# Performance work log

Hardware: AMD Instinct MI355X
Metric: run time of the kernel (lower is better)

The kernel has to match this reference:

```python
import jax, jax.numpy as jnp
import numpy as np

N_NODES = 10000
N_EDGES = 320000
N_GRAPHS = 16


def _sage_layer(h, src, dst, W_self, W_neigh, b):
    # DGL SAGEConv('mean'): out_i = h_i @ W_self + mean_{j in N_in(i)} h_j @ W_neigh + b
    msg_sum = jax.ops.segment_sum(h[src], dst, num_segments=N_NODES)
    deg = jax.ops.segment_sum(jnp.ones(src.shape[0], h.dtype), dst, num_segments=N_NODES)
    h_neigh = msg_sum / jnp.maximum(deg, 1.0)[:, None]
    return h @ W_self + h_neigh @ W_neigh + b


def _segment_mean(x, seg, num_segments):
    s = jax.ops.segment_sum(x, seg, num_segments=num_segments)
    c = jax.ops.segment_sum(jnp.ones(x.shape[0], x.dtype), seg, num_segments=num_segments)
    return s / jnp.maximum(c, 1.0)[:, None]


def setup_inputs() -> dict:
    key = jax.random.key(0)
    ks = jax.random.split(key, 16)
    d_in, d_h, n_cls = 256, 64, 2

    def glorot(k, shape):
        fan_in = shape[0]
        return jax.random.normal(k, shape, dtype=jnp.float32) / np.sqrt(fan_in)

    return {
        "feat": jax.random.normal(ks[0], (N_NODES, d_in), dtype=jnp.float32),
        "src": jax.random.randint(ks[1], (N_EDGES,), 0, N_NODES),
        "dst": jax.random.randint(ks[2], (N_EDGES,), 0, N_NODES),
        "graph_id": jnp.sort(jax.random.randint(ks[3], (N_NODES,), 0, N_GRAPHS)),
        "W_self1": glorot(ks[4], (d_in, d_h)),
        "W_neigh1": glorot(ks[5], (d_in, d_h)),
        "b1": jnp.zeros((d_h,), jnp.float32),
        "W_self2": glorot(ks[6], (d_h, d_h)),
        "W_neigh2": glorot(ks[7], (d_h, d_h)),
        "b2": jnp.zeros((d_h,), jnp.float32),
        "W_self3": glorot(ks[8], (d_h, d_h)),
        "W_neigh3": glorot(ks[9], (d_h, d_h)),
        "b3": jnp.zeros((d_h,), jnp.float32),
        "W_cls": glorot(ks[10], (d_h, n_cls)),
        "b_cls": jnp.zeros((n_cls,), jnp.float32),
    }


def reference(feat, src, dst, graph_id, W_self1, W_neigh1, b1, W_self2, W_neigh2, b2,
              W_self3, W_neigh3, b3, W_cls, b_cls):
    # layer 1 + relu (dropout is identity in eval mode)
    h = jax.nn.relu(_sage_layer(feat, src, dst, W_self1, W_neigh1, b1))
    # layer 2 + relu
    h = jax.nn.relu(_sage_layer(h, src, dst, W_self2, W_neigh2, b2))
    # layer 3 (no activation)
    h = _sage_layer(h, src, dst, W_self3, W_neigh3, b3)
    # dgl.mean_nodes readout per graph
    out_feat = _segment_mean(h, graph_id, N_GRAPHS)
    out = out_feat @ W_cls + b_cls
    return (out, out_feat, h)
```

## Files before the change

kernel.cpp:

```cpp
#include <hip/hip_runtime.h>


#define DH 64
#define NG 16
#define NSB 8
#define DTILES 32
#define MAXNPB 1250
#define CAP 32
#define TILE_F 4352

__device__ __forceinline__ unsigned short f2bf(float f) {
    unsigned int u = __float_as_uint(f);
    unsigned int r = (u + 0x7FFFu + ((u >> 16) & 1u)) >> 16;
    return (unsigned short)r;
}
__device__ __forceinline__ float bfu(unsigned short v) {
    return __uint_as_float(((unsigned int)v) << 16);
}
__device__ __forceinline__ int deg8(const int* __restrict__ cnt8, int n) {
    const int4* cp = reinterpret_cast<const int4*>(&cnt8[n * NSB]);
    int4 c0 = cp[0], c1 = cp[1];
    return c0.x + c0.y + c0.z + c0.w + c1.x + c1.y + c1.z + c1.w;
}

__global__ __launch_bounds__(512) void gemm1_build_kernel(
    const float* __restrict__ X, const float* __restrict__ Ws_g,
    const float* __restrict__ Wn_g, const float* __restrict__ bias,
    float* __restrict__ S, unsigned short* __restrict__ P,
    float* __restrict__ Hn_out,
    const int* __restrict__ src, const int* __restrict__ dst,
    int* __restrict__ cnt8, int* __restrict__ es,
    int M, int E, int npb8, int gb) {
    constexpr int K = 256;
    int tid = threadIdx.x;

    if ((int)blockIdx.x >= gb) {
        int i = ((int)blockIdx.x - gb) * 512 + tid;
        if (i < E) {
            int s = src[i];
            int k = dst[i] * NSB + s / npb8;
            int p = atomicAdd(&cnt8[k], 1);
            if (p < CAP) es[(size_t)k * CAP + p] = s;
        }
        return;
    }

    __shared__ float smem[6 * TILE_F];
    const int grp = tid >> 8;
    const int t   = tid & 255;
    const int cx = t & 15;
    const int ry = t >> 4;
    float* Xs  = smem + grp * 3 * TILE_F;
    float* Wsm = Xs + TILE_F;
    float* Wnm = Wsm + TILE_F;
    const int row0 = blockIdx.x * 64;
    float acc_s[4][4] = {{0.f}};
    float acc_n[4][4] = {{0.f}};

    for (int st = 0; st < 2; ++st) {
        const int kc = grp * 128 + st * 64;
#pragma unroll
        for (int it = 0; it < 4; ++it) {
            int q = t + 256 * it;
            int row = q >> 4;
            int k4 = (q & 15) * 4;
            float4 xv = make_float4(0.f, 0.f, 0.f, 0.f);
            int gr = row0 + row;
            if (gr < M)
                xv = *reinterpret_cast<const float4*>(&X[(size_t)gr * K + kc + k4]);
            *reinterpret_cast<float4*>(&Xs[row * 68 + k4]) = xv;
            *reinterpret_cast<float4*>(&Wsm[row * 68 + k4]) =
                *reinterpret_cast<const float4*>(&Ws_g[(size_t)(kc + row) * 64 + k4]);
            *reinterpret_cast<float4*>(&Wnm[row * 68 + k4]) =
                *reinterpret_cast<const float4*>(&Wn_g[(size_t)(kc + row) * 64 + k4]);
        }
        __syncthreads();
#pragma unroll 4
        for (int kk = 0; kk < 64; ++kk) {
            float av[4], bs[4], bn[4];
#pragma unroll
            for (int j = 0; j < 4; ++j) av[j] = Xs[(ry * 4 + j) * 68 + kk];
#pragma unroll
            for (int i = 0; i < 4; ++i) {
                bs[i] = Wsm[kk * 68 + cx + 16 * i];
                bn[i] = Wnm[kk * 68 + cx + 16 * i];
            }
#pragma unroll
            for (int j = 0; j < 4; ++j)
#pragma unroll
                for (int i = 0; i < 4; ++i) {
                    acc_s[j][i] += av[j] * bs[i];
                    acc_n[j][i] += av[j] * bn[i];
                }
        }
        __syncthreads();
    }

    float* flat = smem + 3 * TILE_F;
    if (grp == 1) {
        int o = t * 33;
#pragma unroll
        for (int j = 0; j < 4; ++j)
#pragma unroll
            for (int i = 0; i < 4; ++i) {
                flat[o + j * 4 + i]      = acc_s[j][i];
                flat[o + 16 + j * 4 + i] = acc_n[j][i];
            }
    }
    __syncthreads();
    if (grp == 0) {
        int o = t * 33;
#pragma unroll
        for (int j = 0; j < 4; ++j)
#pragma unroll
            for (int i = 0; i < 4; ++i) {
                acc_s[j][i] += flat[o + j * 4 + i];
                acc_n[j][i] += flat[o + 16 + j * 4 + i];
            }
#pragma unroll
        for (int j = 0; j < 4; ++j) {
            int r = row0 + ry * 4 + j;
            if (r < M) {
#pragma unroll
                for (int i = 0; i < 4; ++i) {
                    int col = cx + 16 * i;
                    S[(size_t)r * DH + col] = acc_s[j][i] + bias[col];
                    P[(size_t)r * DH + col] = f2bf(acc_n[j][i]);
                    Hn_out[(size_t)r * DH + col] = 0.f;
                }
            }
        }
    }
}

__global__ __launch_bounds__(512) void gemm_dual_kernel(
    const float* __restrict__ X, const float* __restrict__ Ws_g,
    const float* __restrict__ Wn_g, const float* __restrict__ bias,
    const float* __restrict__ Hn_in, const int* __restrict__ cnt8,
    float* __restrict__ S, unsigned short* __restrict__ P,
    float* __restrict__ Hn_out, int M) {
    constexpr int K = 64;
    __shared__ float smem[3 * TILE_F];
    int tid = threadIdx.x;
    const int grp = tid >> 8;
    const int t   = tid & 255;
    const int cx = t & 15;
    const int ry = t >> 4;
    float* Xs  = smem;
    float* Wsm = smem + TILE_F;
    float* Wnm = smem + 2 * TILE_F;
    const int row0 = blockIdx.x * 64;
    float acc_s[4][4] = {{0.f}};
    float acc_n[4][4] = {{0.f}};

    {
#pragma unroll
        for (int it = 0; it < 2; ++it) {
            int q = tid + 512 * it;
            int row = q >> 4;
            int k4 = (q & 15) * 4;
            float4 xv = make_float4(0.f, 0.f, 0.f, 0.f);
            int gr = row0 + row;
            if (gr < M) {
                xv = *reinterpret_cast<const float4*>(&X[(size_t)gr * K + k4]);
                float4 hv = *reinterpret_cast<const float4*>(&Hn_in[(size_t)gr * DH + k4]);
                float inv = 1.f / fmaxf((float)deg8(cnt8, gr), 1.f);
                xv.x = fmaxf(fmaf(hv.x, inv, xv.x), 0.f);
                xv.y = fmaxf(fmaf(hv.y, inv, xv.y), 0.f);
                xv.z = fmaxf(fmaf(hv.z, inv, xv.z), 0.f);
                xv.w = fmaxf(fmaf(hv.w, inv, xv.w), 0.f);
            }
            *reinterpret_cast<float4*>(&Xs[row * 68 + k4]) = xv;
            *reinterpret_cast<float4*>(&Wsm[row * 68 + k4]) =
                *reinterpret_cast<const float4*>(&Ws_g[(size_t)row * 64 + k4]);
            *reinterpret_cast<float4*>(&Wnm[row * 68 + k4]) =
                *reinterpret_cast<const float4*>(&Wn_g[(size_t)row * 64 + k4]);
        }
        __syncthreads();
        const int kk0 = grp * 32;
#pragma unroll 4
        for (int kk = kk0; kk < kk0 + 32; ++kk) {
            float av[4], bs[4], bn[4];
#pragma unroll
            for (int j = 0; j < 4; ++j) av[j] = Xs[(ry * 4 + j) * 68 + kk];
#pragma unroll
            for (int i = 0; i < 4; ++i) {
                bs[i] = Wsm[kk * 68 + cx + 16 * i];
                bn[i] = Wnm[kk * 68 + cx + 16 * i];
            }
#pragma unroll
            for (int j = 0; j < 4; ++j)
#pragma unroll
                for (int i = 0; i < 4; ++i) {
                    acc_s[j][i] += av[j] * bs[i];
                    acc_n[j][i] += av[j] * bn[i];
                }
        }
        __syncthreads();
    }

    if (grp == 1) {
        int o = t * 33;
#pragma unroll
        for (int j = 0; j < 4; ++j)
#pragma unroll
            for (int i = 0; i < 4; ++i) {
                smem[o + j * 4 + i]      = acc_s[j][i];
                smem[o + 16 + j * 4 + i] = acc_n[j][i];
            }
    }
    __syncthreads();
    if (grp == 0) {
        int o = t * 33;
#pragma unroll
        for (int j = 0; j < 4; ++j)
#pragma unroll
            for (int i = 0; i < 4; ++i) {
                acc_s[j][i] += smem[o + j * 4 + i];
                acc_n[j][i] += smem[o + 16 + j * 4 + i];
            }
#pragma unroll
        for (int j = 0; j < 4; ++j) {
            int r = row0 + ry * 4 + j;
            if (r < M) {
#pragma unroll
                for (int i = 0; i < 4; ++i) {
                    int col = cx + 16 * i;
                    S[(size_t)r * DH + col] = acc_s[j][i] + bias[col];
                    P[(size_t)r * DH + col] = f2bf(acc_n[j][i]);
                    Hn_out[(size_t)r * DH + col] = 0.f;
                }
            }
        }
    }
}

__global__ __launch_bounds__(1024) void agg_kernel(
    const unsigned short* __restrict__ P, const int* __restrict__ cnt8,
    const int* __restrict__ es, float* __restrict__ Hn, int M, int npb8) {
    __shared__ __align__(16) unsigned short sP[MAXNPB * DH];
    int tid = threadIdx.x;
    int sb    = blockIdx.x & (NSB - 1);
    int dtile = blockIdx.x >> 3;
    int s0 = sb * npb8;
    int snodes = min(npb8, M - s0);

    {
        const uint4* gp = reinterpret_cast<const uint4*>(P + (size_t)s0 * DH);
        int cnt = snodes * 8;
        for (int j = tid; j < cnt; j += 1024)
            *reinterpret_cast<uint4*>(&sP[j * 8]) = gp[j];
    }
    __syncthreads();

    int lane = tid & 63, wid = tid >> 6;
    int dpb  = (M + DTILES - 1) / DTILES;
    int d0t  = dtile * dpb;
    int dend = min(d0t + dpb, M);

    for (int dstn = d0t + wid; dstn < dend; dstn += 16) {
        int key = dstn * NSB + sb;
        int cnt = min(cnt8[key], CAP);
        if (cnt == 0) continue;
        size_t base = (size_t)key * CAP;
        float acc = 0.f;
        int cmax = cnt - 1;
        for (int e = 0; e < cnt; e += 4) {
            int i0 = es[base + min(e + 0, cmax)] - s0;
            int i1 = es[base + min(e + 1, cmax)] - s0;
            int i2 = es[base + min(e + 2, cmax)] - s0;
            int i3 = es[base + min(e + 3, cmax)] - s0;
            float m1 = (e + 1 < cnt) ? 1.f : 0.f;
            float m2 = (e + 2 < cnt) ? 1.f : 0.f;
            float m3 = (e + 3 < cnt) ? 1.f : 0.f;
            float f0 = bfu(sP[(size_t)i0 * DH + lane]);
            float f1 = bfu(sP[(size_t)i1 * DH + lane]);
            float f2 = bfu(sP[(size_t)i2 * DH + lane]);
            float f3 = bfu(sP[(size_t)i3 * DH + lane]);
            acc += f0;
            acc = fmaf(m1, f1, acc);
            acc = fmaf(m2, f2, acc);
            acc = fmaf(m3, f3, acc);
        }
        atomicAdd(&Hn[(size_t)dstn * DH + lane], acc);
    }
}

__global__ __launch_bounds__(256) void finish_readout_kernel(
    const float* __restrict__ S, const float* __restrict__ Hn,
    const int* __restrict__ cnt8, const int* __restrict__ graph_id,
    float* __restrict__ H, float* __restrict__ gsum, float* __restrict__ gcnt,
    const float* __restrict__ Wc, const float* __restrict__ bc,
    float* __restrict__ out, float* __restrict__ out_feat,
    unsigned int* __restrict__ done, int M, int fb) {
    int tid  = threadIdx.x;
    int lane = tid & 63;
    int wv   = tid >> 6;
    {
        int wid = blockIdx.x * 4 + wv;
        int nw  = fb * 4;
        int cpw = (M + nw - 1) / nw;
        int n0 = wid * cpw, n1 = min(n0 + cpw, M);
        if (n0 < n1) {
            float acc = 0.f;
            int cnt = 0;
            int cur = graph_id[n0];
            for (int n = n0; n < n1; ++n) {
                int gid = graph_id[n];
                if (gid != cur) {
                    atomicAdd(&gsum[cur * DH + lane], acc);
                    if (lane == 0) atomicAdd(&gcnt[cur], (float)cnt);
                    acc = 0.f; cnt = 0; cur = gid;
                }
                float inv = 1.f / fmaxf((float)deg8(cnt8, n), 1.f);
                size_t o = (size_t)n * DH + lane;
                float val = fmaf(Hn[o], inv, S[o]);
                H[o] = val;
                acc += val;
                ++cnt;
            }
            atomicAdd(&gsum[cur * DH + lane], acc);
            if (lane == 0) atomicAdd(&gcnt[cur], (float)cnt);
        }
    }

    __shared__ unsigned int s_ticket;
    __syncthreads();
    if (tid == 0) {
        __threadfence();
        s_ticket = __hip_atomic_fetch_add(done, 1u, __ATOMIC_ACQ_REL,
                                          __HIP_MEMORY_SCOPE_AGENT);
    }
    __syncthreads();
    if (s_ticket != (unsigned int)(fb - 1)) return;
    if (tid == 0) __threadfence();
    __syncthreads();

    __shared__ float ofs[NG][DH];
#pragma unroll
    for (int q = 0; q < 4; ++q) {
        int idx = tid + 256 * q;
        int g = idx >> 6, d = idx & 63;
        float of = gsum[idx] / fmaxf(gcnt[g], 1.0f);
        out_feat[idx] = of;
        ofs[g][d] = of;
    }
    __syncthreads();
    if (tid < NG * 2) {
        int gg = tid >> 1, cc = tid & 1;
        float accv = bc[cc];
#pragma unroll 8
        for (int dd = 0; dd < DH; ++dd) accv += ofs[gg][dd] * Wc[dd * 2 + cc];
        out[gg * 2 + cc] = accv;
    }
}

extern "C" void kernel_launch(void* const* d_in, const int* in_sizes, int n_in,
                              void* d_out, int out_size, void* d_ws, size_t ws_size,
                              hipStream_t stream) {
    const float* feat     = (const float*)d_in[0];
    const int*   src      = (const int*)d_in[1];
    const int*   dst      = (const int*)d_in[2];
    const int*   graph_id = (const int*)d_in[3];
    const float* Ws1 = (const float*)d_in[4];
    const float* Wn1 = (const float*)d_in[5];
    const float* b1  = (const float*)d_in[6];
    const float* Ws2 = (const float*)d_in[7];
    const float* Wn2 = (const float*)d_in[8];
    const float* b2  = (const float*)d_in[9];
    const float* Ws3 = (const float*)d_in[10];
    const float* Wn3 = (const float*)d_in[11];
    const float* b3  = (const float*)d_in[12];
    const float* Wc  = (const float*)d_in[13];
    const float* bc  = (const float*)d_in[14];

    const int M  = in_sizes[3];
    const int E  = in_sizes[1];
    const int M2 = M * NSB;
    const int npb8 = (M + NSB - 1) / NSB;

    float* out      = (float*)d_out;
    float* out_feat = out + NG * 2;
    float* Hbuf     = out_feat + NG * DH;

    char* w = (char*)d_ws;
    size_t off = 0;
    auto carve = [&](size_t bytes) {
        size_t o = off;
        off = (off + bytes + 255) & ~(size_t)255;
        return o;
    };
    int*   cnt8  = (int*)  (w + carve((size_t)M2 * 4));
    float* gsum  = (float*)(w + carve((size_t)NG * DH * 4));
    float* gcnt  = (float*)(w + carve((size_t)NG * 4));
    unsigned int* done = (unsigned int*)(w + carve(4));
    size_t zero_bytes = off;
    int*   es    = (int*)  (w + carve((size_t)M2 * CAP * 4));
    float* Sbuf  = (float*)(w + carve((size_t)M * DH * 4));
    unsigned short* Pbuf = (unsigned short*)(w + carve((size_t)M * DH * 2));
    float* Hn    = (float*)(w + carve((size_t)M * DH * 4));
    (void)ws_size; (void)n_in; (void)out_size;

    (void)hipMemsetAsync(d_ws, 0, zero_bytes, stream);

    int gb = (M + 63) / 64;
    int eb = (E + 511) / 512;
    int ab = NSB * DTILES;
    int fb = 160;

    gemm1_build_kernel<<<gb + eb, 512, 0, stream>>>(
        feat, Ws1, Wn1, b1, Sbuf, Pbuf, Hn,
        src, dst, cnt8, es, M, E, npb8, gb);
    agg_kernel<<<ab, 1024, 0, stream>>>(Pbuf, cnt8, es, Hn, M, npb8);

    gemm_dual_kernel<<<gb, 512, 0, stream>>>(
        Sbuf, Ws2, Wn2, b2, Hn, cnt8, Sbuf, Pbuf, Hn, M);
    agg_kernel<<<ab, 1024, 0, stream>>>(Pbuf, cnt8, es, Hn, M, npb8);

    gemm_dual_kernel<<<gb, 512, 0, stream>>>(
        Sbuf, Ws3, Wn3, b3, Hn, cnt8, Sbuf, Pbuf, Hn, M);
    agg_kernel<<<ab, 1024, 0, stream>>>(Pbuf, cnt8, es, Hn, M, npb8);

    finish_readout_kernel<<<fb, 256, 0, stream>>>(
        Sbuf, Hn, cnt8, graph_id, Hbuf, gsum, gcnt,
        Wc, bc, out, out_feat, done, M, fb);
}
```

Baseline: 233.4 us.

## Replace atomic neighbor accumulation with per-source-bucket partials and 16-bit edge indices

The aggregation kernel now writes one partial sum per (destination, source-bucket) pair with plain stores instead of float atomicAdd into a shared Hn buffer. The consumers (the dual GEMM and the readout) sum the nonzero partials, skipping buckets whose count is zero. This removes the atomics and the zeroing writes of Hn in the GEMM epilogues. Edge source indices are also stored as 16-bit offsets relative to their bucket, halving edge-list traffic. In exchange the partial buffer is eight times larger, and consumers issue up to eight reads per row element.

```diff
diff --git a/kernel.cpp b/kernel.cpp
--- a/kernel.cpp
+++ b/kernel.cpp
@@ -17,19 +17,13 @@
 __device__ __forceinline__ float bfu(unsigned short v) {
     return __uint_as_float(((unsigned int)v) << 16);
 }
-__device__ __forceinline__ int deg8(const int* __restrict__ cnt8, int n) {
-    const int4* cp = reinterpret_cast<const int4*>(&cnt8[n * NSB]);
-    int4 c0 = cp[0], c1 = cp[1];
-    return c0.x + c0.y + c0.z + c0.w + c1.x + c1.y + c1.z + c1.w;
-}
 
 __global__ __launch_bounds__(512) void gemm1_build_kernel(
     const float* __restrict__ X, const float* __restrict__ Ws_g,
     const float* __restrict__ Wn_g, const float* __restrict__ bias,
     float* __restrict__ S, unsigned short* __restrict__ P,
-    float* __restrict__ Hn_out,
     const int* __restrict__ src, const int* __restrict__ dst,
-    int* __restrict__ cnt8, int* __restrict__ es,
+    int* __restrict__ cnt8, unsigned short* __restrict__ es16,
     int M, int E, int npb8, int gb) {
     constexpr int K = 256;
     int tid = threadIdx.x;
@@ -38,9 +32,11 @@
         int i = ((int)blockIdx.x - gb) * 512 + tid;
         if (i < E) {
             int s = src[i];
-            int k = dst[i] * NSB + s / npb8;
+            int b = s / npb8;
+            int k = dst[i] * NSB + b;
             int p = atomicAdd(&cnt8[k], 1);
-            if (p < CAP) es[(size_t)k * CAP + p] = s;
+            if (p < CAP)
+                es16[(size_t)k * CAP + p] = (unsigned short)(s - b * npb8);
         }
         return;
     }
@@ -126,7 +122,6 @@
                     int col = cx + 16 * i;
                     S[(size_t)r * DH + col] = acc_s[j][i] + bias[col];
                     P[(size_t)r * DH + col] = f2bf(acc_n[j][i]);
-                    Hn_out[(size_t)r * DH + col] = 0.f;
                 }
             }
         }
@@ -136,9 +131,8 @@
 __global__ __launch_bounds__(512) void gemm_dual_kernel(
     const float* __restrict__ X, const float* __restrict__ Ws_g,
     const float* __restrict__ Wn_g, const float* __restrict__ bias,
-    const float* __restrict__ Hn_in, const int* __restrict__ cnt8,
-    float* __restrict__ S, unsigned short* __restrict__ P,
-    float* __restrict__ Hn_out, int M) {
+    const float* __restrict__ Hn_part, const int* __restrict__ cnt8,
+    float* __restrict__ S, unsigned short* __restrict__ P, int M) {
     constexpr int K = 64;
     __shared__ float smem[3 * TILE_F];
     int tid = threadIdx.x;
@@ -163,8 +157,21 @@
             int gr = row0 + row;
             if (gr < M) {
                 xv = *reinterpret_cast<const float4*>(&X[(size_t)gr * K + k4]);
-                float4 hv = *reinterpret_cast<const float4*>(&Hn_in[(size_t)gr * DH + k4]);
-                float inv = 1.f / fmaxf((float)deg8(cnt8, gr), 1.f);
+                const int4* cp = reinterpret_cast<const int4*>(&cnt8[gr * NSB]);
+                int4 c0 = cp[0], c1 = cp[1];
+                int ca[8] = {c0.x, c0.y, c0.z, c0.w, c1.x, c1.y, c1.z, c1.w};
+                int deg = ca[0] + ca[1] + ca[2] + ca[3] +
+                          ca[4] + ca[5] + ca[6] + ca[7];
+                float4 hv = make_float4(0.f, 0.f, 0.f, 0.f);
+                size_t pb = (size_t)gr * NSB * DH + k4;
+#pragma unroll
+                for (int b = 0; b < NSB; ++b) {
+                    if (ca[b] > 0) {
+                        float4 pv = *reinterpret_cast<const float4*>(&Hn_part[pb + b * DH]);
+                        hv.x += pv.x; hv.y += pv.y; hv.z += pv.z; hv.w += pv.w;
+                    }
+                }
+                float inv = 1.f / fmaxf((float)deg, 1.f);
                 xv.x = fmaxf(fmaf(hv.x, inv, xv.x), 0.f);
                 xv.y = fmaxf(fmaf(hv.y, inv, xv.y), 0.f);
                 xv.z = fmaxf(fmaf(hv.z, inv, xv.z), 0.f);
@@ -228,7 +235,6 @@
                     int col = cx + 16 * i;
                     S[(size_t)r * DH + col] = acc_s[j][i] + bias[col];
                     P[(size_t)r * DH + col] = f2bf(acc_n[j][i]);
-                    Hn_out[(size_t)r * DH + col] = 0.f;
                 }
             }
         }
@@ -237,7 +243,8 @@
 
 __global__ __launch_bounds__(1024) void agg_kernel(
     const unsigned short* __restrict__ P, const int* __restrict__ cnt8,
-    const int* __restrict__ es, float* __restrict__ Hn, int M, int npb8) {
+    const unsigned short* __restrict__ es16, float* __restrict__ Hn_part,
+    int M, int npb8) {
     __shared__ __align__(16) unsigned short sP[MAXNPB * DH];
     int tid = threadIdx.x;
     int sb    = blockIdx.x & (NSB - 1);
@@ -266,10 +273,10 @@
         float acc = 0.f;
         int cmax = cnt - 1;
         for (int e = 0; e < cnt; e += 4) {
-            int i0 = es[base + min(e + 0, cmax)] - s0;
-            int i1 = es[base + min(e + 1, cmax)] - s0;
-            int i2 = es[base + min(e + 2, cmax)] - s0;
-            int i3 = es[base + min(e + 3, cmax)] - s0;
+            int i0 = es16[base + min(e + 0, cmax)];
+            int i1 = es16[base + min(e + 1, cmax)];
+            int i2 = es16[base + min(e + 2, cmax)];
+            int i3 = es16[base + min(e + 3, cmax)];
             float m1 = (e + 1 < cnt) ? 1.f : 0.f;
             float m2 = (e + 2 < cnt) ? 1.f : 0.f;
             float m3 = (e + 3 < cnt) ? 1.f : 0.f;
@@ -282,12 +289,12 @@
             acc = fmaf(m2, f2, acc);
             acc = fmaf(m3, f3, acc);
         }
-        atomicAdd(&Hn[(size_t)dstn * DH + lane], acc);
+        Hn_part[(size_t)key * DH + lane] = acc;
     }
 }
 
 __global__ __launch_bounds__(256) void finish_readout_kernel(
-    const float* __restrict__ S, const float* __restrict__ Hn,
+    const float* __restrict__ S, const float* __restrict__ Hn_part,
     const int* __restrict__ cnt8, const int* __restrict__ graph_id,
     float* __restrict__ H, float* __restrict__ gsum, float* __restrict__ gcnt,
     const float* __restrict__ Wc, const float* __restrict__ bc,
@@ -312,9 +319,19 @@
                     if (lane == 0) atomicAdd(&gcnt[cur], (float)cnt);
                     acc = 0.f; cnt = 0; cur = gid;
                 }
-                float inv = 1.f / fmaxf((float)deg8(cnt8, n), 1.f);
+                const int4* cp = reinterpret_cast<const int4*>(&cnt8[n * NSB]);
+                int4 c0 = cp[0], c1 = cp[1];
+                int ca[8] = {c0.x, c0.y, c0.z, c0.w, c1.x, c1.y, c1.z, c1.w};
+                int deg = ca[0] + ca[1] + ca[2] + ca[3] +
+                          ca[4] + ca[5] + ca[6] + ca[7];
+                float hn = 0.f;
+                size_t pb = (size_t)n * NSB * DH + lane;
+#pragma unroll
+                for (int b = 0; b < NSB; ++b)
+                    if (ca[b] > 0) hn += Hn_part[pb + b * DH];
+                float inv = 1.f / fmaxf((float)deg, 1.f);
                 size_t o = (size_t)n * DH + lane;
-                float val = fmaf(Hn[o], inv, S[o]);
+                float val = fmaf(hn, inv, S[o]);
                 H[o] = val;
                 acc += val;
                 ++cnt;
@@ -395,10 +412,10 @@
     float* gcnt  = (float*)(w + carve((size_t)NG * 4));
     unsigned int* done = (unsigned int*)(w + carve(4));
     size_t zero_bytes = off;
-    int*   es    = (int*)  (w + carve((size_t)M2 * CAP * 4));
+    unsigned short* es16 = (unsigned short*)(w + carve((size_t)M2 * CAP * 2));
     float* Sbuf  = (float*)(w + carve((size_t)M * DH * 4));
     unsigned short* Pbuf = (unsigned short*)(w + carve((size_t)M * DH * 2));
-    float* Hn    = (float*)(w + carve((size_t)M * DH * 4));
+    float* Hn_part = (float*)(w + carve((size_t)M2 * DH * 4));
     (void)ws_size; (void)n_in; (void)out_size;
 
     (void)hipMemsetAsync(d_ws, 0, zero_bytes, stream);
@@ -409,19 +426,19 @@
     int fb = 160;
 
     gemm1_build_kernel<<<gb + eb, 512, 0, stream>>>(
-        feat, Ws1, Wn1, b1, Sbuf, Pbuf, Hn,
-        src, dst, cnt8, es, M, E, npb8, gb);
-    agg_kernel<<<ab, 1024, 0, stream>>>(Pbuf, cnt8, es, Hn, M, npb8);
+        feat, Ws1, Wn1, b1, Sbuf, Pbuf,
+        src, dst, cnt8, es16, M, E, npb8, gb);
+    agg_kernel<<<ab, 1024, 0, stream>>>(Pbuf, cnt8, es16, Hn_part, M, npb8);
 
     gemm_dual_kernel<<<gb, 512, 0, stream>>>(
-        Sbuf, Ws2, Wn2, b2, Hn, cnt8, Sbuf, Pbuf, Hn, M);
-    agg_kernel<<<ab, 1024, 0, stream>>>(Pbuf, cnt8, es, Hn, M, npb8);
+        Sbuf, Ws2, Wn2, b2, Hn_part, cnt8, Sbuf, Pbuf, M);
+    agg_kernel<<<ab, 1024, 0, stream>>>(Pbuf, cnt8, es16, Hn_part, M, npb8);
 
     gemm_dual_kernel<<<gb, 512, 0, stream>>>(
-        Sbuf, Ws3, Wn3, b3, Hn, cnt8, Sbuf, Pbuf, Hn, M);
-    agg_kernel<<<ab, 1024, 0, stream>>>(Pbuf, cnt8, es, Hn, M, npb8);
+        Sbuf, Ws3, Wn3, b3, Hn_part, cnt8, Sbuf, Pbuf, M);
+    agg_kernel<<<ab, 1024, 0, stream>>>(Pbuf, cnt8, es16, Hn_part, M, npb8);
 
     finish_readout_kernel<<<fb, 256, 0, stream>>>(
-        Sbuf, Hn, cnt8, graph_id, Hbuf, gsum, gcnt,
+        Sbuf, Hn_part, cnt8, graph_id, Hbuf, gsum, gcnt,
         Wc, bc, out, out_feat, done, M, fb);
 }
```

Measured after the change: 259.0 us. +11.0%, slower.

## Fuse aggregation with following GEMM/readout via per-tile dependency counters

Applied to the files above, without the earlier changes.

Merges each aggregation kernel with the next layer's dual GEMM (and the last with the readout) into one launch. Aggregation blocks bump per-destination-tile and per-source-block counters, and GEMM/readout blocks spin on those counters before running. This removes kernel launch boundaries and lets dependent tiles start while other aggregation blocks are still working. The risks are deadlock if waiting blocks are resident before the producers they wait on, a WAR hazard because GEMM overwrites P while other agg blocks may still read it (guarded by pstg), and the extra cost of 1024-thread blocks with 160KB of shared memory for the GEMM role.

```diff
diff --git a/kernel.cpp b/kernel.cpp
--- a/kernel.cpp
+++ b/kernel.cpp
@@ -8,6 +8,10 @@
 #define MAXNPB 1250
 #define CAP 32
 #define TILE_F 4352
+#define FB4 40
+
+#define ACQ_FENCE() __builtin_amdgcn_fence(__ATOMIC_ACQUIRE, "agent")
+#define RLX_LOAD(p) __hip_atomic_load((p), __ATOMIC_RELAXED, __HIP_MEMORY_SCOPE_AGENT)
 
 __device__ __forceinline__ unsigned short f2bf(float f) {
     unsigned int u = __float_as_uint(f);
@@ -133,115 +137,15 @@
     }
 }
 
-__global__ __launch_bounds__(512) void gemm_dual_kernel(
-    const float* __restrict__ X, const float* __restrict__ Ws_g,
-    const float* __restrict__ Wn_g, const float* __restrict__ bias,
-    const float* __restrict__ Hn_in, const int* __restrict__ cnt8,
-    float* __restrict__ S, unsigned short* __restrict__ P,
-    float* __restrict__ Hn_out, int M) {
-    constexpr int K = 64;
-    __shared__ float smem[3 * TILE_F];
+__device__ void agg_role(const unsigned short* __restrict__ P,
+                         const int* __restrict__ cnt8, const int* __restrict__ es,
+                         float* __restrict__ Hn, int M, int npb8, int bid,
+                         int* __restrict__ dtcnt, int* __restrict__ pstg,
+                         char* smemraw) {
+    unsigned short* sP = reinterpret_cast<unsigned short*>(smemraw);
     int tid = threadIdx.x;
-    const int grp = tid >> 8;
-    const int t   = tid & 255;
-    const int cx = t & 15;
-    const int ry = t >> 4;
-    float* Xs  = smem;
-    float* Wsm = smem + TILE_F;
-    float* Wnm = smem + 2 * TILE_F;
-    const int row0 = blockIdx.x * 64;
-    float acc_s[4][4] = {{0.f}};
-    float acc_n[4][4] = {{0.f}};
-
-    {
-#pragma unroll
-        for (int it = 0; it < 2; ++it) {
-            int q = tid + 512 * it;
-            int row = q >> 4;
-            int k4 = (q & 15) * 4;
-            float4 xv = make_float4(0.f, 0.f, 0.f, 0.f);
-            int gr = row0 + row;
-            if (gr < M) {
-                xv = *reinterpret_cast<const float4*>(&X[(size_t)gr * K + k4]);
-                float4 hv = *reinterpret_cast<const float4*>(&Hn_in[(size_t)gr * DH + k4]);
-                float inv = 1.f / fmaxf((float)deg8(cnt8, gr), 1.f);
-                xv.x = fmaxf(fmaf(hv.x, inv, xv.x), 0.f);
-                xv.y = fmaxf(fmaf(hv.y, inv, xv.y), 0.f);
-                xv.z = fmaxf(fmaf(hv.z, inv, xv.z), 0.f);
-                xv.w = fmaxf(fmaf(hv.w, inv, xv.w), 0.f);
-            }
-            *reinterpret_cast<float4*>(&Xs[row * 68 + k4]) = xv;
-            *reinterpret_cast<float4*>(&Wsm[row * 68 + k4]) =
-                *reinterpret_cast<const float4*>(&Ws_g[(size_t)row * 64 + k4]);
-            *reinterpret_cast<float4*>(&Wnm[row * 68 + k4]) =
-                *reinterpret_cast<const float4*>(&Wn_g[(size_t)row * 64 + k4]);
-        }
-        __syncthreads();
-        const int kk0 = grp * 32;
-#pragma unroll 4
-        for (int kk = kk0; kk < kk0 + 32; ++kk) {
-            float av[4], bs[4], bn[4];
-#pragma unroll
-            for (int j = 0; j < 4; ++j) av[j] = Xs[(ry * 4 + j) * 68 + kk];
-#pragma unroll
-            for (int i = 0; i < 4; ++i) {
-                bs[i] = Wsm[kk * 68 + cx + 16 * i];
-                bn[i] = Wnm[kk * 68 + cx + 16 * i];
-            }
-#pragma unroll
-            for (int j = 0; j < 4; ++j)
-#pragma unroll
-                for (int i = 0; i < 4; ++i) {
-                    acc_s[j][i] += av[j] * bs[i];
-                    acc_n[j][i] += av[j] * bn[i];
-                }
-        }
-        __syncthreads();
-    }
-
-    if (grp == 1) {
-        int o = t * 33;
-#pragma unroll
-        for (int j = 0; j < 4; ++j)
-#pragma unroll
-            for (int i = 0; i < 4; ++i) {
-                smem[o + j * 4 + i]      = acc_s[j][i];
-                smem[o + 16 + j * 4 + i] = acc_n[j][i];
-            }
-    }
-    __syncthreads();
-    if (grp == 0) {
-        int o = t * 33;
-#pragma unroll
-        for (int j = 0; j < 4; ++j)
-#pragma unroll
-            for (int i = 0; i < 4; ++i) {
-                acc_s[j][i] += smem[o + j * 4 + i];
-                acc_n[j][i] += smem[o + 16 + j * 4 + i];
-            }
-#pragma unroll
-        for (int j = 0; j < 4; ++j) {
-            int r = row0 + ry * 4 + j;
-            if (r < M) {
-#pragma unroll
-                for (int i = 0; i < 4; ++i) {
-                    int col = cx + 16 * i;
-                    S[(size_t)r * DH + col] = acc_s[j][i] + bias[col];
-                    P[(size_t)r * DH + col] = f2bf(acc_n[j][i]);
-                    Hn_out[(size_t)r * DH + col] = 0.f;
-                }
-            }
-        }
-    }
-}
-
-__global__ __launch_bounds__(1024) void agg_kernel(
-    const unsigned short* __restrict__ P, const int* __restrict__ cnt8,
-    const int* __restrict__ es, float* __restrict__ Hn, int M, int npb8) {
-    __shared__ __align__(16) unsigned short sP[MAXNPB * DH];
-    int tid = threadIdx.x;
-    int sb    = blockIdx.x & (NSB - 1);
-    int dtile = blockIdx.x >> 3;
+    int sb    = bid & (NSB - 1);
+    int dtile = bid >> 3;
     int s0 = sb * npb8;
     int snodes = min(npb8, M - s0);
 
@@ -252,6 +156,8 @@
             *reinterpret_cast<uint4*>(&sP[j * 8]) = gp[j];
     }
     __syncthreads();
+    if (tid == 0)
+        __hip_atomic_fetch_add(&pstg[sb], 1, __ATOMIC_RELAXED, __HIP_MEMORY_SCOPE_AGENT);
 
     int lane = tid & 63, wid = tid >> 6;
     int dpb  = (M + DTILES - 1) / DTILES;
@@ -284,21 +190,180 @@
         }
         atomicAdd(&Hn[(size_t)dstn * DH + lane], acc);
     }
-}
-
-__global__ __launch_bounds__(256) void finish_readout_kernel(
-    const float* __restrict__ S, const float* __restrict__ Hn,
-    const int* __restrict__ cnt8, const int* __restrict__ graph_id,
+    __syncthreads();
+    if (tid == 0) {
+        __threadfence();
+        __hip_atomic_fetch_add(&dtcnt[dtile], 1, __ATOMIC_RELAXED, __HIP_MEMORY_SCOPE_AGENT);
+    }
+}
+
+__device__ void gemm_role(const float* __restrict__ Ws_g,
+                          const float* __restrict__ Wn_g,
+                          const float* __restrict__ bias,
+                          const int* __restrict__ cnt8,
+                          float* __restrict__ S, unsigned short* __restrict__ P,
+                          float* __restrict__ Hn, int M, int npb8, int tile,
+                          int* __restrict__ dtcnt, int* __restrict__ pstg,
+                          char* smemraw) {
+    float* smem = reinterpret_cast<float*>(smemraw);
+    int tid = threadIdx.x;
+    const int row0 = tile * 64;
+    const int dpb = (M + DTILES - 1) / DTILES;
+
+    if (tid == 0) {
+        int d0 = row0 / dpb, d1 = min((row0 + 63) / dpb, DTILES - 1);
+        int b0 = row0 / npb8, b1 = min((row0 + 63) / npb8, NSB - 1);
+        while (RLX_LOAD(&dtcnt[d0]) < NSB) __builtin_amdgcn_s_sleep(8);
+        if (d1 != d0)
+            while (RLX_LOAD(&dtcnt[d1]) < NSB) __builtin_amdgcn_s_sleep(8);
+        while (RLX_LOAD(&pstg[b0]) < DTILES) __builtin_amdgcn_s_sleep(8);
+        if (b1 != b0)
+            while (RLX_LOAD(&pstg[b1]) < DTILES) __builtin_amdgcn_s_sleep(8);
+        ACQ_FENCE();
+    }
+    __syncthreads();
+
+    const int grp = tid >> 8;
+    const int t   = tid & 255;
+    const int cx = t & 15;
+    const int ry = t >> 4;
+    float* Xs  = smem;
+    float* Wsm = smem + TILE_F;
+    float* Wnm = smem + 2 * TILE_F;
+    float acc_s[4][4] = {{0.f}};
+    float acc_n[4][4] = {{0.f}};
+
+    if (tid < 512) {
+#pragma unroll
+        for (int it = 0; it < 2; ++it) {
+            int q = tid + 512 * it;
+            int row = q >> 4;
+            int k4 = (q & 15) * 4;
+            float4 xv = make_float4(0.f, 0.f, 0.f, 0.f);
+            int gr = row0 + row;
+            if (gr < M) {
+                xv = *reinterpret_cast<const float4*>(&S[(size_t)gr * DH + k4]);
+                float4 hv = *reinterpret_cast<const float4*>(&Hn[(size_t)gr * DH + k4]);
+                float inv = 1.f / fmaxf((float)deg8(cnt8, gr), 1.f);
+                xv.x = fmaxf(fmaf(hv.x, inv, xv.x), 0.f);
+                xv.y = fmaxf(fmaf(hv.y, inv, xv.y), 0.f);
+                xv.z = fmaxf(fmaf(hv.z, inv, xv.z), 0.f);
+                xv.w = fmaxf(fmaf(hv.w, inv, xv.w), 0.f);
+            }
+            *reinterpret_cast<float4*>(&Xs[row * 68 + k4]) = xv;
+            *reinterpret_cast<float4*>(&Wsm[row * 68 + k4]) =
+                *reinterpret_cast<const float4*>(&Ws_g[(size_t)row * 64 + k4]);
+            *reinterpret_cast<float4*>(&Wnm[row * 68 + k4]) =
+                *reinterpret_cast<const float4*>(&Wn_g[(size_t)row * 64 + k4]);
+        }
+    }
+    __syncthreads();
+    if (tid < 512) {
+        const int kk0 = grp * 32;
+#pragma unroll 4
+        for (int kk = kk0; kk < kk0 + 32; ++kk) {
+            float av[4], bs[4], bn[4];
+#pragma unroll
+            for (int j = 0; j < 4; ++j) av[j] = Xs[(ry * 4 + j) * 68 + kk];
+#pragma unroll
+            for (int i = 0; i < 4; ++i) {
+                bs[i] = Wsm[kk * 68 + cx + 16 * i];
+                bn[i] = Wnm[kk * 68 + cx + 16 * i];
+            }
+#pragma unroll
+            for (int j = 0; j < 4; ++j)
+#pragma unroll
+                for (int i = 0; i < 4; ++i) {
+                    acc_s[j][i] += av[j] * bs[i];
+                    acc_n[j][i] += av[j] * bn[i];
+                }
+        }
+    }
+    __syncthreads();
+
+    if (tid < 512 && (tid >> 8) == 1) {
+        int o = t * 33;
+#pragma unroll
+        for (int j = 0; j < 4; ++j)
+#pragma unroll
+            for (int i = 0; i < 4; ++i) {
+                smem[o + j * 4 + i]      = acc_s[j][i];
+                smem[o + 16 + j * 4 + i] = acc_n[j][i];
+            }
+    }
+    __syncthreads();
+    if (tid < 256) {
+        int o = t * 33;
+#pragma unroll
+        for (int j = 0; j < 4; ++j)
+#pragma unroll
+            for (int i = 0; i < 4; ++i) {
+                acc_s[j][i] += smem[o + j * 4 + i];
+                acc_n[j][i] += smem[o + 16 + j * 4 + i];
+            }
+#pragma unroll
+        for (int j = 0; j < 4; ++j) {
+            int r = row0 + ry * 4 + j;
+            if (r < M) {
+#pragma unroll
+                for (int i = 0; i < 4; ++i) {
+                    int col = cx + 16 * i;
+                    S[(size_t)r * DH + col] = acc_s[j][i] + bias[col];
+                    P[(size_t)r * DH + col] = f2bf(acc_n[j][i]);
+                    Hn[(size_t)r * DH + col] = 0.f;
+                }
+            }
+        }
+    }
+}
+
+__global__ __launch_bounds__(1024) void agg_gemm_kernel(
+    unsigned short* __restrict__ P, const int* __restrict__ cnt8,
+    const int* __restrict__ es, float* __restrict__ Hn,
+    const float* __restrict__ Ws_g, const float* __restrict__ Wn_g,
+    const float* __restrict__ bias, float* __restrict__ S,
+    int* __restrict__ dtcnt, int* __restrict__ pstg,
+    int M, int npb8, int ab) {
+    __shared__ __align__(16) char smemraw[160000];
+    if ((int)blockIdx.x < ab)
+        agg_role(P, cnt8, es, Hn, M, npb8, blockIdx.x, dtcnt, pstg, smemraw);
+    else
+        gemm_role(Ws_g, Wn_g, bias, cnt8, S, P, Hn, M, npb8,
+                  blockIdx.x - ab, dtcnt, pstg, smemraw);
+}
+
+__global__ __launch_bounds__(1024) void agg_finish_kernel(
+    unsigned short* __restrict__ P, const int* __restrict__ cnt8,
+    const int* __restrict__ es, float* __restrict__ Hn,
+    const float* __restrict__ S, const int* __restrict__ graph_id,
     float* __restrict__ H, float* __restrict__ gsum, float* __restrict__ gcnt,
     const float* __restrict__ Wc, const float* __restrict__ bc,
     float* __restrict__ out, float* __restrict__ out_feat,
-    unsigned int* __restrict__ done, int M, int fb) {
-    int tid  = threadIdx.x;
-    int lane = tid & 63;
-    int wv   = tid >> 6;
+    unsigned int* __restrict__ done, int* __restrict__ dtcnt,
+    int* __restrict__ pstg, int M, int npb8, int ab) {
+    __shared__ __align__(16) char smemraw[160000];
+    int tid = threadIdx.x;
+    if ((int)blockIdx.x < ab) {
+        agg_role(P, cnt8, es, Hn, M, npb8, blockIdx.x, dtcnt, pstg, smemraw);
+        return;
+    }
+    int fbid = blockIdx.x - ab;
+    int dpb = (M + DTILES - 1) / DTILES;
+    if (tid == 0) {
+        int nlo = fbid * 256;
+        int d0 = min(nlo / dpb, DTILES - 1);
+        int d1 = min((nlo + 255) / dpb, DTILES - 1);
+        while (RLX_LOAD(&dtcnt[d0]) < NSB) __builtin_amdgcn_s_sleep(8);
+        if (d1 != d0)
+            while (RLX_LOAD(&dtcnt[d1]) < NSB) __builtin_amdgcn_s_sleep(8);
+        ACQ_FENCE();
+    }
+    __syncthreads();
+
+    int lane = tid & 63, wvl = tid >> 6;
     {
-        int wid = blockIdx.x * 4 + wv;
-        int nw  = fb * 4;
+        int wid = fbid * 16 + wvl;
+        int nw  = FB4 * 16;
         int cpw = (M + nw - 1) / nw;
         int n0 = wid * cpw, n1 = min(n0 + cpw, M);
         if (n0 < n1) {
@@ -324,33 +389,31 @@
         }
     }
 
-    __shared__ unsigned int s_ticket;
+    float* ofs = reinterpret_cast<float*>(smemraw);
+    unsigned int* s_ticket = reinterpret_cast<unsigned int*>(smemraw + NG * DH * 4);
     __syncthreads();
     if (tid == 0) {
         __threadfence();
-        s_ticket = __hip_atomic_fetch_add(done, 1u, __ATOMIC_ACQ_REL,
-                                          __HIP_MEMORY_SCOPE_AGENT);
-    }
-    __syncthreads();
-    if (s_ticket != (unsigned int)(fb - 1)) return;
+        *s_ticket = __hip_atomic_fetch_add(done, 1u, __ATOMIC_ACQ_REL,
+                                           __HIP_MEMORY_SCOPE_AGENT);
+    }
+    __syncthreads();
+    if (*s_ticket != (unsigned int)(FB4 - 1)) return;
     if (tid == 0) __threadfence();
     __syncthreads();
 
-    __shared__ float ofs[NG][DH];
-#pragma unroll
-    for (int q = 0; q < 4; ++q) {
-        int idx = tid + 256 * q;
-        int g = idx >> 6, d = idx & 63;
-        float of = gsum[idx] / fmaxf(gcnt[g], 1.0f);
-        out_feat[idx] = of;
-        ofs[g][d] = of;
+    {
+        int g = tid >> 6;
+        float of = gsum[tid] / fmaxf(gcnt[g], 1.0f);
+        out_feat[tid] = of;
+        ofs[tid] = of;
     }
     __syncthreads();
     if (tid < NG * 2) {
         int gg = tid >> 1, cc = tid & 1;
         float accv = bc[cc];
 #pragma unroll 8
-        for (int dd = 0; dd < DH; ++dd) accv += ofs[gg][dd] * Wc[dd * 2 + cc];
+        for (int dd = 0; dd < DH; ++dd) accv += ofs[gg * DH + dd] * Wc[dd * 2 + cc];
         out[gg * 2 + cc] = accv;
     }
 }
@@ -394,6 +457,12 @@
     float* gsum  = (float*)(w + carve((size_t)NG * DH * 4));
     float* gcnt  = (float*)(w + carve((size_t)NG * 4));
     unsigned int* done = (unsigned int*)(w + carve(4));
+    int*   dt1   = (int*)  (w + carve(DTILES * 4));
+    int*   dt2   = (int*)  (w + carve(DTILES * 4));
+    int*   dt3   = (int*)  (w + carve(DTILES * 4));
+    int*   ps1   = (int*)  (w + carve(NSB * 4));
+    int*   ps2   = (int*)  (w + carve(NSB * 4));
+    int*   ps3   = (int*)  (w + carve(NSB * 4));
     size_t zero_bytes = off;
     int*   es    = (int*)  (w + carve((size_t)M2 * CAP * 4));
     float* Sbuf  = (float*)(w + carve((size_t)M * DH * 4));
@@ -406,22 +475,18 @@
     int gb = (M + 63) / 64;
     int eb = (E + 511) / 512;
     int ab = NSB * DTILES;
-    int fb = 160;
 
     gemm1_build_kernel<<<gb + eb, 512, 0, stream>>>(
         feat, Ws1, Wn1, b1, Sbuf, Pbuf, Hn,
         src, dst, cnt8, es, M, E, npb8, gb);
-    agg_kernel<<<ab, 1024, 0, stream>>>(Pbuf, cnt8, es, Hn, M, npb8);
-
-    gemm_dual_kernel<<<gb, 512, 0, stream>>>(
-        Sbuf, Ws2, Wn2, b2, Hn, cnt8, Sbuf, Pbuf, Hn, M);
-    agg_kernel<<<ab, 1024, 0, stream>>>(Pbuf, cnt8, es, Hn, M, npb8);
-
-    gemm_dual_kernel<<<gb, 512, 0, stream>>>(
-        Sbuf, Ws3, Wn3, b3, Hn, cnt8, Sbuf, Pbuf, Hn, M);
-    agg_kernel<<<ab, 1024, 0, stream>>>(Pbuf, cnt8, es, Hn, M, npb8);
-
-    finish_readout_kernel<<<fb, 256, 0, stream>>>(
-        Sbuf, Hn, cnt8, graph_id, Hbuf, gsum, gcnt,
-        Wc, bc, out, out_feat, done, M, fb);
-}
+
+    agg_gemm_kernel<<<ab + gb, 1024, 0, stream>>>(
+        Pbuf, cnt8, es, Hn, Ws2, Wn2, b2, Sbuf, dt1, ps1, M, npb8, ab);
+
+    agg_gemm_kernel<<<ab + gb, 1024, 0, stream>>>(
+        Pbuf, cnt8, es, Hn, Ws3, Wn3, b3, Sbuf, dt2, ps2, M, npb8, ab);
+
+    agg_finish_kernel<<<ab + FB4, 1024, 0, stream>>>(
+        Pbuf, cnt8, es, Hn, Sbuf, graph_id, Hbuf, gsum, gcnt,
+        Wc, bc, out, out_feat, done, dt3, ps3, M, npb8, ab);
+}
```

New measurement: 257.0 us. 10.1% more time.
